# Performance work log

Measured on AMD Instinct MI355X. Metric: run time of the kernel, lower is better.

The kernel has to match this reference:

```python
import jax, jax.numpy as jnp
import numpy as np

HEAD_DEPTH = 64
CLIP = 10.0
SCALE = float(np.sqrt(HEAD_DEPTH))


def setup_inputs() -> dict:
    key = jax.random.key(0)
    kq, kk, kv, km = jax.random.split(key, 4)
    B, H, S, D = 4, 16, 2048, HEAD_DEPTH
    q = jax.random.normal(kq, (B, H, S, D), dtype=jnp.float32)
    k = jax.random.normal(kk, (B, H, S, D), dtype=jnp.float32)
    v = jax.random.normal(kv, (B, H, S, D), dtype=jnp.float32)
    # mask: (batch, n_nodes, 1) bool; True => key position is masked out
    mask = jax.random.randint(km, (B, S, 1), 0, 2).astype(bool)
    return {"q": q, "k": k, "v": v, "mask": mask}


def reference(q, k, v, mask):
    # logits: (B, H, Sq, Sk)
    logits = jnp.einsum('bhqd,bhkd->bhqk', q, k) / SCALE
    logits = CLIP * jnp.tanh(logits)  # tanh-clip of logits
    # mask (B, N, 1) -> broadcast over heads and query positions: (B, 1, 1, N)
    key_mask = mask[:, None, None, :, 0]
    logits = jnp.where(key_mask, -jnp.inf, logits)
    probs = jax.nn.softmax(logits, axis=-1)
    return jnp.einsum('bhqk,bhkd->bhqd', probs, v)
```

## Files before the change

### kernel.cpp

```cpp
#include <hip/hip_runtime.h>

typedef short bf16x8 __attribute__((ext_vector_type(8), may_alias));
typedef float f32x4 __attribute__((ext_vector_type(4)));
typedef unsigned int u32x4a __attribute__((ext_vector_type(4), may_alias));
typedef unsigned int u32x2a __attribute__((ext_vector_type(2), may_alias));
typedef unsigned short ushort;
typedef unsigned int uint;

#define B_N 4
#define H_N 16
#define S_N 2048
#define D_N 64
#define BQ 128
#define WQ 32
#define KT 64
#define NW 4
#define NBLK (B_N*H_N*(S_N/BQ))
#define TILE_BYTES 32768
#define MAXTILE (S_N/KT)
#define IMG_OFF 32768
#define WS_NEED ((size_t)IMG_OFF + (size_t)B_N*H_N*MAXTILE*TILE_BYTES)

#define MFMA16 __builtin_amdgcn_mfma_f32_16x16x32_bf16

__device__ __forceinline__ uint f2bf(float x){
  uint u = __float_as_uint(x);
  u += 0x7fffu + ((u >> 16) & 1u);
  return u >> 16;
}
__device__ __forceinline__ float bf2f(uint h){
  return __uint_as_float(h << 16);
}
__device__ __forceinline__ int ldsw(int off, int row){
  return off ^ ((row & 7) << 4);
}
__device__ __forceinline__ void gload16(const void* g, void* l){
  __builtin_amdgcn_global_load_lds((const uint __attribute__((address_space(1)))*)g,
                                   (uint __attribute__((address_space(3)))*)l, 16, 0, 0);
}

__global__ __launch_bounds__(256)
void compact_k(const int* __restrict__ Mg, int* __restrict__ cnt_ws,
               ushort* __restrict__ idx_ws)
{
  __shared__ int sws[NW];
  const int b = blockIdx.x;
  const int tid = threadIdx.x, lane = tid & 63, w = tid >> 6;
  const int* mb = Mg + (size_t)b * S_N;
  int kept[8]; int cl = 0; int base = tid * 8;
  #pragma unroll
  for (int i = 0; i < 8; ++i){ kept[i] = (mb[base+i] == 0); cl += kept[i]; }
  int inc = cl;
  #pragma unroll
  for (int d = 1; d < 64; d <<= 1){
    int o = __shfl_up(inc, d);
    if (lane >= d) inc += o;
  }
  if (lane == 63) sws[w] = inc;
  __syncthreads();
  int s0 = sws[0], s1 = sws[1], s2 = sws[2], s3 = sws[3];
  int wo = (w > 0 ? s0 : 0) + (w > 1 ? s1 : 0) + (w > 2 ? s2 : 0);
  int pos = wo + inc - cl;
  #pragma unroll
  for (int i = 0; i < 8; ++i){
    if (kept[i]) idx_ws[b*S_N + pos++] = (ushort)(base + i);
  }
  if (tid == 0) cnt_ws[b] = s0 + s1 + s2 + s3;
}

__global__ __launch_bounds__(256)
void stage_k(const float* __restrict__ Kg, const float* __restrict__ Vg,
             const int* __restrict__ cnt_ws, const ushort* __restrict__ idx_ws,
             char* __restrict__ img)
{
  __shared__ float Vl[64*65];
  const int bid = blockIdx.x;
  const int bh = bid >> 5;
  const int tile = bid & 31;
  const int b = bh >> 4;
  const int cnt = cnt_ws[b];
  const int ntile = (cnt + 63) >> 6;
  if (tile >= ntile) return;
  const int tid = threadIdx.x;
  char* G = img + (size_t)bid * TILE_BYTES;

  const int jrow = tid >> 2, c4 = tid & 3;
  int kk = tile*64 + jrow; if (kk >= cnt) kk = cnt - 1;
  const int sidx = idx_ws[b*S_N + kk];
  const size_t kvbase = (size_t)bh * (size_t)(S_N*D_N);
  const int sw = (jrow & 7) << 4;
  {
    const float4* Kp = (const float4*)(Kg + kvbase + (size_t)sidx*D_N) + c4*4;
    float4 k0 = Kp[0], k1 = Kp[1], k2 = Kp[2], k3 = Kp[3];
    float kv[16] = {k0.x,k0.y,k0.z,k0.w,k1.x,k1.y,k1.z,k1.w,
                    k2.x,k2.y,k2.z,k2.w,k3.x,k3.y,k3.z,k3.w};
    uint h[16], l[16];
    #pragma unroll
    for (int e = 0; e < 16; ++e){
      uint hh = f2bf(kv[e]); h[e] = hh; l[e] = f2bf(kv[e] - bf2f(hh));
    }
    char* r0 = G + jrow*128;
    char* r1 = G + 8192 + jrow*128;
    *(u32x4a*)(r0 + ((c4*32)      ^ sw)) = (u32x4a){h[0]|(h[1]<<16),  h[2]|(h[3]<<16),
                                                    h[4]|(h[5]<<16),  h[6]|(h[7]<<16)};
    *(u32x4a*)(r0 + ((c4*32 + 16) ^ sw)) = (u32x4a){h[8]|(h[9]<<16),  h[10]|(h[11]<<16),
                                                    h[12]|(h[13]<<16),h[14]|(h[15]<<16)};
    *(u32x4a*)(r1 + ((c4*32)      ^ sw)) = (u32x4a){l[0]|(l[1]<<16),  l[2]|(l[3]<<16),
                                                    l[4]|(l[5]<<16),  l[6]|(l[7]<<16)};
    *(u32x4a*)(r1 + ((c4*32 + 16) ^ sw)) = (u32x4a){l[8]|(l[9]<<16),  l[10]|(l[11]<<16),
                                                    l[12]|(l[13]<<16),l[14]|(l[15]<<16)};
  }
  {
    const float4* Vp = (const float4*)(Vg + kvbase + (size_t)sidx*D_N) + c4*4;
    float4 v0 = Vp[0], v1 = Vp[1], v2 = Vp[2], v3 = Vp[3];
    float vv[16] = {v0.x,v0.y,v0.z,v0.w,v1.x,v1.y,v1.z,v1.w,
                    v2.x,v2.y,v2.z,v2.w,v3.x,v3.y,v3.z,v3.w};
    #pragma unroll
    for (int e = 0; e < 16; ++e) Vl[jrow*65 + c4*16 + e] = vv[e];
  }
  __syncthreads();
  #pragma unroll
  for (int t = 0; t < 2; ++t){
    int idx2 = tid + t*256;
    int d = idx2 >> 3;
    int h = (idx2 >> 2) & 1;
    int g = idx2 & 3;
    int kb = h*32 + g*4;
    uint hh[8], ll[8];
    #pragma unroll
    for (int e = 0; e < 8; ++e){
      int k = kb + (e & 3) + ((e >> 2) << 4);
      float x = Vl[k*65 + d];
      uint hv = f2bf(x); hh[e] = hv; ll[e] = f2bf(x - bf2f(hv));
    }
    *(u32x4a*)(G + 16384 + d*128 + h*64 + g*16) =
        (u32x4a){hh[0]|(hh[1]<<16), hh[2]|(hh[3]<<16), hh[4]|(hh[5]<<16), hh[6]|(hh[7]<<16)};
    *(u32x4a*)(G + 24576 + d*128 + h*64 + g*16) =
        (u32x4a){ll[0]|(ll[1]<<16), ll[2]|(ll[3]<<16), ll[4]|(ll[5]<<16), ll[6]|(ll[7]<<16)};
  }
}

__global__ __launch_bounds__(256, 2)
void attn5_k(const float* __restrict__ Qg, const char* __restrict__ img,
             const int* __restrict__ cnt_ws, float* __restrict__ Og)
{
  __shared__ __align__(16) char smem[2][16384];

  const int tid  = threadIdx.x;
  const int lane = tid & 63;
  const int w    = tid >> 6;
  const int c    = lane & 15;
  const int gi   = lane >> 4;

  int bid = blockIdx.x;
  int wg  = (bid & 7) * (NBLK/8) + (bid >> 3);
  int qt  = wg & 15;
  int bh  = wg >> 4;
  int b   = bh >> 4;

  const int cnt = cnt_ws[b];
  const int nhalf = (cnt + 31) >> 5;
  const char* Gb = img + (size_t)bh * MAXTILE * TILE_BYTES;

  auto stage = [&](int hidx, int sb){
    const char* T = Gb + (size_t)(hidx >> 1) * TILE_BYTES;
    const int h = hidx & 1;
    char* Bse = (char*)&smem[sb][0];
    if (w < 2){
      const char* src = T + w*8192 + h*4096 + lane*16;
      char* dst = Bse + w*4096;
      #pragma unroll
      for (int i = 0; i < 4; ++i) gload16(src + i*1024, dst + i*1024);
    } else {
      const int hl = w - 2;
      const char* base = T + 16384 + hl*8192 + h*64;
      char* dst = Bse + 8192 + hl*4096;
      #pragma unroll
      for (int i = 0; i < 4; ++i){
        int pos = i*1024 + lane*16;
        int d = pos >> 6;
        int g = (pos >> 4) & 3;
        gload16(base + d*128 + g*16, dst + i*1024);
      }
    }
  };

  if (nhalf > 0) stage(0, 0);

  const int q0w = qt * BQ + w * WQ;
  bf16x8 qh[2][2], ql[2][2];
  {
    const float* Qbase = Qg + (size_t)bh * S_N * D_N;
    #pragma unroll
    for (int qs = 0; qs < 2; ++qs){
      const float* qr = Qbase + (size_t)(q0w + qs*16 + c) * D_N;
      #pragma unroll
      for (int ks = 0; ks < 2; ++ks){
        const float4* p4 = (const float4*)(qr + ks*32 + gi*8);
        float4 x0 = p4[0], x1 = p4[1];
        float xs[8] = {x0.x,x0.y,x0.z,x0.w,x1.x,x1.y,x1.z,x1.w};
        union { bf16x8 v; ushort u[8]; } uh, ul;
        #pragma unroll
        for (int e = 0; e < 8; ++e){
          uint h = f2bf(xs[e]);
          uh.u[e] = (ushort)h;
          ul.u[e] = (ushort)f2bf(xs[e] - bf2f(h));
        }
        qh[qs][ks] = uh.v; ql[qs][ks] = ul.v;
      }
    }
  }

  f32x4 Oa[2][4];
  #pragma unroll
  for (int i = 0; i < 2; ++i)
    #pragma unroll
    for (int jj = 0; jj < 4; ++jj)
      Oa[i][jj] = (f32x4){0.f,0.f,0.f,0.f};
  float zz[2] = {0.f, 0.f};

  const int swc16 = (c & 7) << 4;
  const int e0 = (gi*16) ^ swc16;
  const int e1 = (64 + gi*16) ^ swc16;

  __syncthreads();

  for (int tb = 0; tb < nhalf; ++tb){
    const int buf = tb & 1;
    if (tb + 1 < nhalf) stage(tb + 1, buf ^ 1);
    const char* Khi  = &smem[buf][0];
    const char* Klo  = Khi + 4096;
    const char* VThi = Khi + 8192;
    const char* VTlo = Khi + 12288;
    const bool lastt = (tb == nhalf - 1);

    uint sH[2][4], sL[2][4];
    #pragma unroll
    for (int kt = 0; kt < 2; ++kt){
      int row = kt*16 + c;
      const char* krh = Khi + row*128;
      const char* krl = Klo + row*128;
      bf16x8 kh0 = *(const bf16x8*)(krh + e0);
      bf16x8 kh1 = *(const bf16x8*)(krh + e1);
      bf16x8 kl0 = *(const bf16x8*)(krl + e0);
      bf16x8 kl1 = *(const bf16x8*)(krl + e1);
      #pragma unroll
      for (int qs = 0; qs < 2; ++qs){
        f32x4 s = (f32x4){0.f,0.f,0.f,0.f};
        s = MFMA16(kh0, qh[qs][0], s, 0,0,0);
        s = MFMA16(kh1, qh[qs][1], s, 0,0,0);
        s = MFMA16(kh0, ql[qs][0], s, 0,0,0);
        s = MFMA16(kh1, ql[qs][1], s, 0,0,0);
        s = MFMA16(kl0, qh[qs][0], s, 0,0,0);
        s = MFMA16(kl1, qh[qs][1], s, 0,0,0);
        float pv[4];
        #pragma unroll
        for (int r = 0; r < 4; ++r){
          float t  = __builtin_amdgcn_exp2f(s[r] * 0.3606737602222409f);
          float wv = __builtin_amdgcn_rcpf(t + 1.0f);
          pv[r] = __builtin_amdgcn_exp2f(-28.853900817779268f * wv);
        }
        if (lastt){
          int kg0 = tb*32 + kt*16 + gi*4;
          #pragma unroll
          for (int r = 0; r < 4; ++r) if (kg0 + r >= cnt) pv[r] = 0.f;
        }
        zz[qs] += (pv[0] + pv[1]) + (pv[2] + pv[3]);
        uint hA, hB, lA, lB;
        asm("v_cvt_pk_bf16_f32 %0, %1, %2" : "=v"(hA) : "v"(pv[0]), "v"(pv[1]));
        asm("v_cvt_pk_bf16_f32 %0, %1, %2" : "=v"(hB) : "v"(pv[2]), "v"(pv[3]));
        float l0 = pv[0] - __uint_as_float(hA << 16);
        float l1 = pv[1] - __uint_as_float(hA & 0xffff0000u);
        float l2 = pv[2] - __uint_as_float(hB << 16);
        float l3 = pv[3] - __uint_as_float(hB & 0xffff0000u);
        asm("v_cvt_pk_bf16_f32 %0, %1, %2" : "=v"(lA) : "v"(l0), "v"(l1));
        asm("v_cvt_pk_bf16_f32 %0, %1, %2" : "=v"(lB) : "v"(l2), "v"(l3));
        sH[qs][kt*2+0] = hA; sH[qs][kt*2+1] = hB;
        sL[qs][kt*2+0] = lA; sL[qs][kt*2+1] = lB;
      }
    }
    union PU { u32x4a g; bf16x8 v; };
    PU pah[2], pal[2];
    #pragma unroll
    for (int qs = 0; qs < 2; ++qs){
      pah[qs].g = (u32x4a){sH[qs][0], sH[qs][1], sH[qs][2], sH[qs][3]};
      pal[qs].g = (u32x4a){sL[qs][0], sL[qs][1], sL[qs][2], sL[qs][3]};
    }
    #pragma unroll
    for (int ds = 0; ds < 4; ++ds){
      int drow = ds*16 + c;
      bf16x8 vh = *(const bf16x8*)(VThi + drow*64 + gi*16);
      bf16x8 vl = *(const bf16x8*)(VTlo + drow*64 + gi*16);
      #pragma unroll
      for (int qs = 0; qs < 2; ++qs){
        f32x4 o = Oa[qs][ds];
        o = MFMA16(pah[qs].v, vh, o, 0,0,0);
        o = MFMA16(pah[qs].v, vl, o, 0,0,0);
        o = MFMA16(pal[qs].v, vh, o, 0,0,0);
        Oa[qs][ds] = o;
      }
    }
    __syncthreads();
  }

  #pragma unroll
  for (int qs = 0; qs < 2; ++qs){
    float zt = zz[qs];
    zt += __shfl_xor(zt, 16);
    zt += __shfl_xor(zt, 32);
    float rz = 1.0f / zt;
    #pragma unroll
    for (int r = 0; r < 4; ++r){
      float rzq = __shfl(rz, gi*4 + r);
      size_t rowbase = ((size_t)bh * S_N + (size_t)(q0w + qs*16 + gi*4 + r)) * D_N;
      #pragma unroll
      for (int ds = 0; ds < 4; ++ds){
        Og[rowbase + ds*16 + c] = Oa[qs][ds][r] * rzq;
      }
    }
  }
}

__global__ __launch_bounds__(256, 2)
void attn_k(const float* __restrict__ Qg, const float* __restrict__ Kg,
            const float* __restrict__ Vg, const int* __restrict__ Mg,
            float* __restrict__ Og)
{
  __shared__ __align__(16) ushort Khi[KT*D_N];
  __shared__ __align__(16) ushort Klo[KT*D_N];
  __shared__ __align__(16) ushort Vhi[D_N*72];
  __shared__ __align__(16) ushort Vlo[D_N*72];
  __shared__ __align__(16) ushort Phl[NW*16*72];
  __shared__ __align__(16) ushort Pll[NW*16*72];
  __shared__ ushort idx_l[S_N];
  __shared__ int scan_ws[NW];

  const int tid  = threadIdx.x;
  const int lane = tid & 63;
  const int w    = tid >> 6;
  const int c    = lane & 15;
  const int gi   = lane >> 4;

  int bid = blockIdx.x;
  int wg  = (bid & 7) * (NBLK/8) + (bid >> 3);
  int qt  = wg & 15;
  int bh  = wg >> 4;
  int b   = bh >> 4;

  int cnt;
  {
    const int* mb = Mg + (size_t)b * S_N;
    int kept[8]; int cl = 0;
    int base = tid * 8;
    #pragma unroll
    for (int i = 0; i < 8; ++i){ kept[i] = (mb[base+i] == 0); cl += kept[i]; }
    int inc = cl;
    #pragma unroll
    for (int d = 1; d < 64; d <<= 1){
      int o = __shfl_up(inc, d);
      if (lane >= d) inc += o;
    }
    if (lane == 63) scan_ws[w] = inc;
    __syncthreads();
    int s0 = scan_ws[0], s1 = scan_ws[1], s2 = scan_ws[2], s3 = scan_ws[3];
    int wo = (w > 0 ? s0 : 0) + (w > 1 ? s1 : 0) + (w > 2 ? s2 : 0);
    cnt = s0 + s1 + s2 + s3;
    int pos = wo + inc - cl;
    #pragma unroll
    for (int i = 0; i < 8; ++i){
      if (kept[i]) idx_l[pos++] = (ushort)(base + i);
    }
    __syncthreads();
  }

  const int q0w = qt * BQ + w * WQ;
  bf16x8 qh[2][2], ql[2][2];
  {
    const float* Qbase = Qg + (size_t)bh * S_N * D_N;
    #pragma unroll
    for (int qs = 0; qs < 2; ++qs){
      const float* qr = Qbase + (size_t)(q0w + qs*16 + c) * D_N;
      #pragma unroll
      for (int ks = 0; ks < 2; ++ks){
        const float4* p4 = (const float4*)(qr + ks*32 + gi*8);
        float4 x0 = p4[0], x1 = p4[1];
        float xs[8] = {x0.x,x0.y,x0.z,x0.w,x1.x,x1.y,x1.z,x1.w};
        union { bf16x8 v; ushort u[8]; } uh, ul;
        #pragma unroll
        for (int e = 0; e < 8; ++e){
          uint h = f2bf(xs[e]);
          uh.u[e] = (ushort)h;
          ul.u[e] = (ushort)f2bf(xs[e] - bf2f(h));
        }
        qh[qs][ks] = uh.v; ql[qs][ks] = ul.v;
      }
    }
  }

  f32x4 Oa[2][4];
  #pragma unroll
  for (int i = 0; i < 2; ++i)
    #pragma unroll
    for (int jj = 0; jj < 4; ++jj)
      Oa[i][jj] = (f32x4){0.f,0.f,0.f,0.f};
  float zz[2] = {0.f, 0.f};

  ushort* Ph = Phl + w * (16*72);
  ushort* Pl = Pll + w * (16*72);

  const int jrow = tid >> 2;
  const int c4   = tid & 3;
  const size_t kvbase = (size_t)bh * S_N * D_N;

  const int ntile = (cnt + KT - 1) >> 6;
  for (int tb = 0; tb < ntile; ++tb){
    {
      int kk = tb*KT + jrow;
      int ci = kk < cnt ? kk : cnt - 1;
      int sidx = idx_l[ci];
      const float4* Kp = (const float4*)(Kg + kvbase + (size_t)sidx * D_N) + c4*4;
      const float4* Vp = (const float4*)(Vg + kvbase + (size_t)sidx * D_N) + c4*4;
      float4 k0 = Kp[0], k1 = Kp[1], k2 = Kp[2], k3 = Kp[3];
      float kv[16] = {k0.x,k0.y,k0.z,k0.w,k1.x,k1.y,k1.z,k1.w,
                      k2.x,k2.y,k2.z,k2.w,k3.x,k3.y,k3.z,k3.w};
      uint kh[16], klv[16];
      #pragma unroll
      for (int e = 0; e < 16; ++e){
        uint h = f2bf(kv[e]);
        kh[e] = h; klv[e] = f2bf(kv[e] - bf2f(h));
      }
      u32x4a H0 = (u32x4a){kh[0]|(kh[1]<<16),   kh[2]|(kh[3]<<16),
                           kh[4]|(kh[5]<<16),   kh[6]|(kh[7]<<16)};
      u32x4a H1 = (u32x4a){kh[8]|(kh[9]<<16),   kh[10]|(kh[11]<<16),
                           kh[12]|(kh[13]<<16), kh[14]|(kh[15]<<16)};
      u32x4a L0 = (u32x4a){klv[0]|(klv[1]<<16),   klv[2]|(klv[3]<<16),
                           klv[4]|(klv[5]<<16),   klv[6]|(klv[7]<<16)};
      u32x4a L1 = (u32x4a){klv[8]|(klv[9]<<16),   klv[10]|(klv[11]<<16),
                           klv[12]|(klv[13]<<16), klv[14]|(klv[15]<<16)};
      char* krh = (char*)Khi + jrow*128;
      char* krl = (char*)Klo + jrow*128;
      int o0 = ldsw(c4*32, jrow), o1 = ldsw(c4*32 + 16, jrow);
      *(u32x4a*)(krh + o0) = H0;  *(u32x4a*)(krh + o1) = H1;
      *(u32x4a*)(krl + o0) = L0;  *(u32x4a*)(krl + o1) = L1;

      float4 v0 = Vp[0], v1 = Vp[1], v2 = Vp[2], v3 = Vp[3];
      float vv[16] = {v0.x,v0.y,v0.z,v0.w,v1.x,v1.y,v1.z,v1.w,
                      v2.x,v2.y,v2.z,v2.w,v3.x,v3.y,v3.z,v3.w};
      #pragma unroll
      for (int e = 0; e < 16; ++e){
        int d = c4*16 + e;
        uint h  = f2bf(vv[e]);
        uint l2 = f2bf(vv[e] - bf2f(h));
        int off = d*144 + ldsw(jrow*2, d);
        *(ushort*)((char*)Vhi + off) = (ushort)h;
        *(ushort*)((char*)Vlo + off) = (ushort)l2;
      }
    }
    __syncthreads();

    const bool lastt = (tb == ntile - 1);
    #pragma unroll
    for (int qs = 0; qs < 2; ++qs){
      #pragma unroll
      for (int kt = 0; kt < 4; ++kt){
        int row = kt*16 + c;
        const char* krh = (const char*)Khi + row*128;
        const char* krl = (const char*)Klo + row*128;
        int e0 = ldsw(16*gi, row), e1 = ldsw(64 + 16*gi, row);
        bf16x8 kh0 = *(const bf16x8*)(krh + e0);
        bf16x8 kh1 = *(const bf16x8*)(krh + e1);
        bf16x8 kl0 = *(const bf16x8*)(krl + e0);
        bf16x8 kl1 = *(const bf16x8*)(krl + e1);
        f32x4 s = (f32x4){0.f,0.f,0.f,0.f};
        s = MFMA16(kh0, qh[qs][0], s, 0,0,0);
        s = MFMA16(kh1, qh[qs][1], s, 0,0,0);
        s = MFMA16(kh0, ql[qs][0], s, 0,0,0);
        s = MFMA16(kh1, ql[qs][1], s, 0,0,0);
        s = MFMA16(kl0, qh[qs][0], s, 0,0,0);
        s = MFMA16(kl1, qh[qs][1], s, 0,0,0);
        float pv[4];
        #pragma unroll
        for (int r = 0; r < 4; ++r){
          float t  = __builtin_amdgcn_exp2f(s[r] * 0.3606737602222409f);
          float wv = __builtin_amdgcn_rcpf(t + 1.0f);
          pv[r] = __builtin_amdgcn_exp2f(-28.853900817779268f * wv);
        }
        if (lastt){
          int kg0 = tb*KT + kt*16 + gi*4;
          #pragma unroll
          for (int r = 0; r < 4; ++r) if (kg0 + r >= cnt) pv[r] = 0.f;
        }
        zz[qs] += (pv[0] + pv[1]) + (pv[2] + pv[3]);
        uint h0 = f2bf(pv[0]), h1 = f2bf(pv[1]),
             h2 = f2bf(pv[2]), h3 = f2bf(pv[3]);
        uint l0 = f2bf(pv[0]-bf2f(h0)), l1 = f2bf(pv[1]-bf2f(h1)),
             l2 = f2bf(pv[2]-bf2f(h2)), l3 = f2bf(pv[3]-bf2f(h3));
        int ow = c*144 + ldsw(kt*32 + gi*8, c);
        *(u32x2a*)((char*)Ph + ow) = (u32x2a){h0|(h1<<16), h2|(h3<<16)};
        *(u32x2a*)((char*)Pl + ow) = (u32x2a){l0|(l1<<16), l2|(l3<<16)};
      }
      bf16x8 pah[2], pal[2];
      {
        const char* prh = (const char*)Ph + c*144;
        const char* prl = (const char*)Pl + c*144;
        #pragma unroll
        for (int ks = 0; ks < 2; ++ks){
          int oo = ldsw(64*ks + 16*gi, c);
          pah[ks] = *(const bf16x8*)(prh + oo);
          pal[ks] = *(const bf16x8*)(prl + oo);
        }
      }
      #pragma unroll
      for (int ds = 0; ds < 4; ++ds){
        int drow = ds*16 + c;
        const char* vrh = (const char*)Vhi + drow*144;
        const char* vrl = (const char*)Vlo + drow*144;
        f32x4 o = Oa[qs][ds];
        #pragma unroll
        for (int ks = 0; ks < 2; ++ks){
          int oo = ldsw(64*ks + 16*gi, drow);
          bf16x8 vh = *(const bf16x8*)(vrh + oo);
          bf16x8 vl = *(const bf16x8*)(vrl + oo);
          o = MFMA16(pah[ks], vh, o, 0,0,0);
          o = MFMA16(pah[ks], vl, o, 0,0,0);
          o = MFMA16(pal[ks], vh, o, 0,0,0);
        }
        Oa[qs][ds] = o;
      }
    }
    __syncthreads();
  }

  #pragma unroll
  for (int qs = 0; qs < 2; ++qs){
    float zt = zz[qs];
    zt += __shfl_xor(zt, 16);
    zt += __shfl_xor(zt, 32);
    float rz = 1.0f / zt;
    #pragma unroll
    for (int r = 0; r < 4; ++r){
      float rzq = __shfl(rz, gi*4 + r);
      size_t rowbase = ((size_t)bh * S_N + (size_t)(q0w + qs*16 + gi*4 + r)) * D_N;
      #pragma unroll
      for (int ds = 0; ds < 4; ++ds){
        Og[rowbase + ds*16 + c] = Oa[qs][ds][r] * rzq;
      }
    }
  }
}

extern "C" void kernel_launch(void* const* d_in, const int* in_sizes, int n_in,
                              void* d_out, int out_size, void* d_ws, size_t ws_size,
                              hipStream_t stream) {
  const float* Qg = (const float*)d_in[0];
  const float* Kg = (const float*)d_in[1];
  const float* Vg = (const float*)d_in[2];
  const int*   Mg = (const int*)d_in[3];
  float* Og = (float*)d_out;
  if (ws_size >= WS_NEED){
    int*    cnt_ws = (int*)d_ws;
    ushort* idx_ws = (ushort*)((char*)d_ws + 64);
    char*   img    = (char*)d_ws + IMG_OFF;
    compact_k<<<dim3(B_N), dim3(256), 0, stream>>>(Mg, cnt_ws, idx_ws);
    stage_k<<<dim3(B_N*H_N*MAXTILE), dim3(256), 0, stream>>>(Kg, Vg, cnt_ws, idx_ws, img);
    attn5_k<<<dim3(NBLK), dim3(256), 0, stream>>>(Qg, img, cnt_ws, Og);
  } else {
    attn_k<<<dim3(NBLK), dim3(256), 0, stream>>>(Qg, Kg, Vg, Mg, Og);
  }
}
```

Baseline: 137.2 us.

## Read K/V fragments directly from global in MFMA-ready layout, drop LDS staging

The staged K/V image is rewritten into a fragment-major layout, so each lane's bf16x8 MFMA operand sits contiguously and a wave's loads are coalesced 16-byte reads. The attention kernel then loads K and V fragments straight from global memory (relying on L2/cache reuse across the 4 waves and 16 query tiles) instead of double-buffering through LDS with global_load_lds and per-tile barriers. This removes LDS traffic and the __syncthreads, at the cost of each wave issuing its own global loads, with latency no longer hidden by async prefetch.

```diff
diff --git a/kernel.cpp b/kernel.cpp
--- a/kernel.cpp
+++ b/kernel.cpp
@@ -33,10 +33,6 @@
 }
 __device__ __forceinline__ int ldsw(int off, int row){
   return off ^ ((row & 7) << 4);
-}
-__device__ __forceinline__ void gload16(const void* g, void* l){
-  __builtin_amdgcn_global_load_lds((const uint __attribute__((address_space(1)))*)g,
-                                   (uint __attribute__((address_space(3)))*)l, 16, 0, 0);
 }
 
 __global__ __launch_bounds__(256)
@@ -88,7 +84,6 @@
   int kk = tile*64 + jrow; if (kk >= cnt) kk = cnt - 1;
   const int sidx = idx_ws[b*S_N + kk];
   const size_t kvbase = (size_t)bh * (size_t)(S_N*D_N);
-  const int sw = (jrow & 7) << 4;
   {
     const float4* Kp = (const float4*)(Kg + kvbase + (size_t)sidx*D_N) + c4*4;
     float4 k0 = Kp[0], k1 = Kp[1], k2 = Kp[2], k3 = Kp[3];
@@ -99,16 +94,15 @@
     for (int e = 0; e < 16; ++e){
       uint hh = f2bf(kv[e]); h[e] = hh; l[e] = f2bf(kv[e] - bf2f(hh));
     }
-    char* r0 = G + jrow*128;
-    char* r1 = G + 8192 + jrow*128;
-    *(u32x4a*)(r0 + ((c4*32)      ^ sw)) = (u32x4a){h[0]|(h[1]<<16),  h[2]|(h[3]<<16),
-                                                    h[4]|(h[5]<<16),  h[6]|(h[7]<<16)};
-    *(u32x4a*)(r0 + ((c4*32 + 16) ^ sw)) = (u32x4a){h[8]|(h[9]<<16),  h[10]|(h[11]<<16),
-                                                    h[12]|(h[13]<<16),h[14]|(h[15]<<16)};
-    *(u32x4a*)(r1 + ((c4*32)      ^ sw)) = (u32x4a){l[0]|(l[1]<<16),  l[2]|(l[3]<<16),
-                                                    l[4]|(l[5]<<16),  l[6]|(l[7]<<16)};
-    *(u32x4a*)(r1 + ((c4*32 + 16) ^ sw)) = (u32x4a){l[8]|(l[9]<<16),  l[10]|(l[11]<<16),
-                                                    l[12]|(l[13]<<16),l[14]|(l[15]<<16)};
+    const int g0 = c4*2, g1 = c4*2 + 1;
+    *(u32x4a*)(G + g0*1024 + jrow*16) = (u32x4a){h[0]|(h[1]<<16),  h[2]|(h[3]<<16),
+                                                 h[4]|(h[5]<<16),  h[6]|(h[7]<<16)};
+    *(u32x4a*)(G + g1*1024 + jrow*16) = (u32x4a){h[8]|(h[9]<<16),  h[10]|(h[11]<<16),
+                                                 h[12]|(h[13]<<16),h[14]|(h[15]<<16)};
+    *(u32x4a*)(G + 8192 + g0*1024 + jrow*16) = (u32x4a){l[0]|(l[1]<<16),  l[2]|(l[3]<<16),
+                                                        l[4]|(l[5]<<16),  l[6]|(l[7]<<16)};
+    *(u32x4a*)(G + 8192 + g1*1024 + jrow*16) = (u32x4a){l[8]|(l[9]<<16),  l[10]|(l[11]<<16),
+                                                        l[12]|(l[13]<<16),l[14]|(l[15]<<16)};
   }
   {
     const float4* Vp = (const float4*)(Vg + kvbase + (size_t)sidx*D_N) + c4*4;
@@ -133,19 +127,17 @@
       float x = Vl[k*65 + d];
       uint hv = f2bf(x); hh[e] = hv; ll[e] = f2bf(x - bf2f(hv));
     }
-    *(u32x4a*)(G + 16384 + d*128 + h*64 + g*16) =
+    *(u32x4a*)(G + 16384 + g*2048 + h*1024 + d*16) =
         (u32x4a){hh[0]|(hh[1]<<16), hh[2]|(hh[3]<<16), hh[4]|(hh[5]<<16), hh[6]|(hh[7]<<16)};
-    *(u32x4a*)(G + 24576 + d*128 + h*64 + g*16) =
+    *(u32x4a*)(G + 24576 + g*2048 + h*1024 + d*16) =
         (u32x4a){ll[0]|(ll[1]<<16), ll[2]|(ll[3]<<16), ll[4]|(ll[5]<<16), ll[6]|(ll[7]<<16)};
   }
 }
 
 __global__ __launch_bounds__(256, 2)
-void attn5_k(const float* __restrict__ Qg, const char* __restrict__ img,
+void attn6_k(const float* __restrict__ Qg, const char* __restrict__ img,
              const int* __restrict__ cnt_ws, float* __restrict__ Og)
 {
-  __shared__ __align__(16) char smem[2][16384];
-
   const int tid  = threadIdx.x;
   const int lane = tid & 63;
   const int w    = tid >> 6;
@@ -161,31 +153,6 @@
   const int cnt = cnt_ws[b];
   const int nhalf = (cnt + 31) >> 5;
   const char* Gb = img + (size_t)bh * MAXTILE * TILE_BYTES;
-
-  auto stage = [&](int hidx, int sb){
-    const char* T = Gb + (size_t)(hidx >> 1) * TILE_BYTES;
-    const int h = hidx & 1;
-    char* Bse = (char*)&smem[sb][0];
-    if (w < 2){
-      const char* src = T + w*8192 + h*4096 + lane*16;
-      char* dst = Bse + w*4096;
-      #pragma unroll
-      for (int i = 0; i < 4; ++i) gload16(src + i*1024, dst + i*1024);
-    } else {
-      const int hl = w - 2;
-      const char* base = T + 16384 + hl*8192 + h*64;
-      char* dst = Bse + 8192 + hl*4096;
-      #pragma unroll
-      for (int i = 0; i < 4; ++i){
-        int pos = i*1024 + lane*16;
-        int d = pos >> 6;
-        int g = (pos >> 4) & 3;
-        gload16(base + d*128 + g*16, dst + i*1024);
-      }
-    }
-  };
-
-  if (nhalf > 0) stage(0, 0);
 
   const int q0w = qt * BQ + w * WQ;
   bf16x8 qh[2][2], ql[2][2];
@@ -219,31 +186,19 @@
       Oa[i][jj] = (f32x4){0.f,0.f,0.f,0.f};
   float zz[2] = {0.f, 0.f};
 
-  const int swc16 = (c & 7) << 4;
-  const int e0 = (gi*16) ^ swc16;
-  const int e1 = (64 + gi*16) ^ swc16;
-
-  __syncthreads();
-
   for (int tb = 0; tb < nhalf; ++tb){
-    const int buf = tb & 1;
-    if (tb + 1 < nhalf) stage(tb + 1, buf ^ 1);
-    const char* Khi  = &smem[buf][0];
-    const char* Klo  = Khi + 4096;
-    const char* VThi = Khi + 8192;
-    const char* VTlo = Khi + 12288;
+    const char* T  = Gb + (size_t)(tb >> 1) * TILE_BYTES;
+    const char* KB = T + gi*1024 + ((tb & 1)*32 + c)*16;
+    const char* VB = T + 16384 + gi*2048 + (tb & 1)*1024 + c*16;
     const bool lastt = (tb == nhalf - 1);
 
     uint sH[2][4], sL[2][4];
     #pragma unroll
     for (int kt = 0; kt < 2; ++kt){
-      int row = kt*16 + c;
-      const char* krh = Khi + row*128;
-      const char* krl = Klo + row*128;
-      bf16x8 kh0 = *(const bf16x8*)(krh + e0);
-      bf16x8 kh1 = *(const bf16x8*)(krh + e1);
-      bf16x8 kl0 = *(const bf16x8*)(krl + e0);
-      bf16x8 kl1 = *(const bf16x8*)(krl + e1);
+      bf16x8 kh0 = *(const bf16x8*)(KB + kt*256);
+      bf16x8 kh1 = *(const bf16x8*)(KB + 4096 + kt*256);
+      bf16x8 kl0 = *(const bf16x8*)(KB + 8192 + kt*256);
+      bf16x8 kl1 = *(const bf16x8*)(KB + 12288 + kt*256);
       #pragma unroll
       for (int qs = 0; qs < 2; ++qs){
         f32x4 s = (f32x4){0.f,0.f,0.f,0.f};
@@ -288,9 +243,8 @@
     }
     #pragma unroll
     for (int ds = 0; ds < 4; ++ds){
-      int drow = ds*16 + c;
-      bf16x8 vh = *(const bf16x8*)(VThi + drow*64 + gi*16);
-      bf16x8 vl = *(const bf16x8*)(VTlo + drow*64 + gi*16);
+      bf16x8 vh = *(const bf16x8*)(VB + ds*256);
+      bf16x8 vl = *(const bf16x8*)(VB + 8192 + ds*256);
       #pragma unroll
       for (int qs = 0; qs < 2; ++qs){
         f32x4 o = Oa[qs][ds];
@@ -300,7 +254,6 @@
         Oa[qs][ds] = o;
       }
     }
-    __syncthreads();
   }
 
   #pragma unroll
@@ -563,7 +516,7 @@
     char*   img    = (char*)d_ws + IMG_OFF;
     compact_k<<<dim3(B_N), dim3(256), 0, stream>>>(Mg, cnt_ws, idx_ws);
     stage_k<<<dim3(B_N*H_N*MAXTILE), dim3(256), 0, stream>>>(Kg, Vg, cnt_ws, idx_ws, img);
-    attn5_k<<<dim3(NBLK), dim3(256), 0, stream>>>(Qg, img, cnt_ws, Og);
+    attn6_k<<<dim3(NBLK), dim3(256), 0, stream>>>(Qg, img, cnt_ws, Og);
   } else {
     attn_k<<<dim3(NBLK), dim3(256), 0, stream>>>(Qg, Kg, Vg, Mg, Og);
   }
```

Result: slower. 149.2 us (+8.8%).

## Read V operands directly from global memory in MFMA layout, skip LDS staging

Applied to the files above, without the earlier changes.

The staging kernel now writes V^T hi/lo into a layout that matches the per-lane MFMA operand order. The attention kernel then loads V fragments straight from global memory (through cache) instead of copying them into shared memory. Only K is double-buffered in LDS, which halves shared memory per block and removes half of the async copies. The cost is that V loads become global-latency reads inside the inner loop with no prefetch, and every wave re-reads the same V data from cache.

```diff
diff --git a/kernel.cpp b/kernel.cpp
--- a/kernel.cpp
+++ b/kernel.cpp
@@ -133,18 +133,18 @@
       float x = Vl[k*65 + d];
       uint hv = f2bf(x); hh[e] = hv; ll[e] = f2bf(x - bf2f(hv));
     }
-    *(u32x4a*)(G + 16384 + d*128 + h*64 + g*16) =
+    *(u32x4a*)(G + 16384 + g*2048 + h*1024 + d*16) =
         (u32x4a){hh[0]|(hh[1]<<16), hh[2]|(hh[3]<<16), hh[4]|(hh[5]<<16), hh[6]|(hh[7]<<16)};
-    *(u32x4a*)(G + 24576 + d*128 + h*64 + g*16) =
+    *(u32x4a*)(G + 24576 + g*2048 + h*1024 + d*16) =
         (u32x4a){ll[0]|(ll[1]<<16), ll[2]|(ll[3]<<16), ll[4]|(ll[5]<<16), ll[6]|(ll[7]<<16)};
   }
 }
 
 __global__ __launch_bounds__(256, 2)
-void attn5_k(const float* __restrict__ Qg, const char* __restrict__ img,
+void attn9_k(const float* __restrict__ Qg, const char* __restrict__ img,
              const int* __restrict__ cnt_ws, float* __restrict__ Og)
 {
-  __shared__ __align__(16) char smem[2][16384];
+  __shared__ __align__(16) char smem[2][8192];
 
   const int tid  = threadIdx.x;
   const int lane = tid & 63;
@@ -163,25 +163,13 @@
   const char* Gb = img + (size_t)bh * MAXTILE * TILE_BYTES;
 
   auto stage = [&](int hidx, int sb){
-    const char* T = Gb + (size_t)(hidx >> 1) * TILE_BYTES;
-    const int h = hidx & 1;
-    char* Bse = (char*)&smem[sb][0];
     if (w < 2){
+      const char* T = Gb + (size_t)(hidx >> 1) * TILE_BYTES;
+      const int h = hidx & 1;
       const char* src = T + w*8192 + h*4096 + lane*16;
-      char* dst = Bse + w*4096;
+      char* dst = (char*)&smem[sb][0] + w*4096;
       #pragma unroll
       for (int i = 0; i < 4; ++i) gload16(src + i*1024, dst + i*1024);
-    } else {
-      const int hl = w - 2;
-      const char* base = T + 16384 + hl*8192 + h*64;
-      char* dst = Bse + 8192 + hl*4096;
-      #pragma unroll
-      for (int i = 0; i < 4; ++i){
-        int pos = i*1024 + lane*16;
-        int d = pos >> 6;
-        int g = (pos >> 4) & 3;
-        gload16(base + d*128 + g*16, dst + i*1024);
-      }
     }
   };
 
@@ -230,8 +218,8 @@
     if (tb + 1 < nhalf) stage(tb + 1, buf ^ 1);
     const char* Khi  = &smem[buf][0];
     const char* Klo  = Khi + 4096;
-    const char* VThi = Khi + 8192;
-    const char* VTlo = Khi + 12288;
+    const char* VB = Gb + (size_t)(tb >> 1) * TILE_BYTES + 16384
+                     + gi*2048 + (tb & 1)*1024 + c*16;
     const bool lastt = (tb == nhalf - 1);
 
     uint sH[2][4], sL[2][4];
@@ -288,9 +276,8 @@
     }
     #pragma unroll
     for (int ds = 0; ds < 4; ++ds){
-      int drow = ds*16 + c;
-      bf16x8 vh = *(const bf16x8*)(VThi + drow*64 + gi*16);
-      bf16x8 vl = *(const bf16x8*)(VTlo + drow*64 + gi*16);
+      bf16x8 vh = *(const bf16x8*)(VB + ds*256);
+      bf16x8 vl = *(const bf16x8*)(VB + 8192 + ds*256);
       #pragma unroll
       for (int qs = 0; qs < 2; ++qs){
         f32x4 o = Oa[qs][ds];
@@ -563,7 +550,7 @@
     char*   img    = (char*)d_ws + IMG_OFF;
     compact_k<<<dim3(B_N), dim3(256), 0, stream>>>(Mg, cnt_ws, idx_ws);
     stage_k<<<dim3(B_N*H_N*MAXTILE), dim3(256), 0, stream>>>(Kg, Vg, cnt_ws, idx_ws, img);
-    attn5_k<<<dim3(NBLK), dim3(256), 0, stream>>>(Qg, img, cnt_ws, Og);
+    attn9_k<<<dim3(NBLK), dim3(256), 0, stream>>>(Qg, img, cnt_ws, Og);
   } else {
     attn_k<<<dim3(NBLK), dim3(256), 0, stream>>>(Qg, Kg, Vg, Mg, Og);
   }
```

Measured after the change: 167.6 us. +22.1%, slower.

## Process full 64-key tiles per iteration with swizzled V^T staging in LDS

Applied to the files above, without the earlier changes.

The attention loop now consumes a whole 64-key staged tile per iteration instead of a 32-key half tile. This halves the number of loop trips and barriers, and each staging call issues twice as many async global-to-LDS loads. The V^T copy is XOR-swizzled on load so the wider 128-byte rows avoid LDS bank conflicts. Shared memory per block doubles to 64KB, and the score and packed-probability register arrays double, which may limit occupancy or cause spills under the 2-blocks launch bound. Masking of the last partial tile now uses 64-key granularity, so more wasted work on the tail.

```diff
diff --git a/kernel.cpp b/kernel.cpp
--- a/kernel.cpp
+++ b/kernel.cpp
@@ -141,10 +141,10 @@
 }
 
 __global__ __launch_bounds__(256, 2)
-void attn5_k(const float* __restrict__ Qg, const char* __restrict__ img,
-             const int* __restrict__ cnt_ws, float* __restrict__ Og)
+void attn13_k(const float* __restrict__ Qg, const char* __restrict__ img,
+              const int* __restrict__ cnt_ws, float* __restrict__ Og)
 {
-  __shared__ __align__(16) char smem[2][16384];
+  __shared__ __align__(16) char smem[2][32768];
 
   const int tid  = threadIdx.x;
   const int lane = tid & 63;
@@ -159,33 +159,32 @@
   int b   = bh >> 4;
 
   const int cnt = cnt_ws[b];
-  const int nhalf = (cnt + 31) >> 5;
+  const int ntile = (cnt + 63) >> 6;
   const char* Gb = img + (size_t)bh * MAXTILE * TILE_BYTES;
 
-  auto stage = [&](int hidx, int sb){
-    const char* T = Gb + (size_t)(hidx >> 1) * TILE_BYTES;
-    const int h = hidx & 1;
+  auto stage = [&](int t, int sb){
+    const char* T = Gb + (size_t)t * TILE_BYTES;
     char* Bse = (char*)&smem[sb][0];
     if (w < 2){
-      const char* src = T + w*8192 + h*4096 + lane*16;
-      char* dst = Bse + w*4096;
-      #pragma unroll
-      for (int i = 0; i < 4; ++i) gload16(src + i*1024, dst + i*1024);
+      const char* src = T + w*8192 + lane*16;
+      char* dst = Bse + w*8192;
+      #pragma unroll
+      for (int i = 0; i < 8; ++i) gload16(src + i*1024, dst + i*1024);
     } else {
       const int hl = w - 2;
-      const char* base = T + 16384 + hl*8192 + h*64;
-      char* dst = Bse + 8192 + hl*4096;
-      #pragma unroll
-      for (int i = 0; i < 4; ++i){
+      const char* base = T + 16384 + hl*8192;
+      char* dst = Bse + 16384 + hl*8192;
+      #pragma unroll
+      for (int i = 0; i < 8; ++i){
         int pos = i*1024 + lane*16;
-        int d = pos >> 6;
-        int g = (pos >> 4) & 3;
-        gload16(base + d*128 + g*16, dst + i*1024);
+        int d = pos >> 7;
+        int off = pos & 127;
+        gload16(base + d*128 + (off ^ ((d & 7) << 4)), dst + i*1024);
       }
     }
   };
 
-  if (nhalf > 0) stage(0, 0);
+  if (ntile > 0) stage(0, 0);
 
   const int q0w = qt * BQ + w * WQ;
   bf16x8 qh[2][2], ql[2][2];
@@ -225,18 +224,18 @@
 
   __syncthreads();
 
-  for (int tb = 0; tb < nhalf; ++tb){
+  for (int tb = 0; tb < ntile; ++tb){
     const int buf = tb & 1;
-    if (tb + 1 < nhalf) stage(tb + 1, buf ^ 1);
+    if (tb + 1 < ntile) stage(tb + 1, buf ^ 1);
     const char* Khi  = &smem[buf][0];
-    const char* Klo  = Khi + 4096;
-    const char* VThi = Khi + 8192;
-    const char* VTlo = Khi + 12288;
-    const bool lastt = (tb == nhalf - 1);
-
-    uint sH[2][4], sL[2][4];
-    #pragma unroll
-    for (int kt = 0; kt < 2; ++kt){
+    const char* Klo  = Khi + 8192;
+    const char* VThi = Khi + 16384;
+    const char* VTlo = Khi + 24576;
+    const bool lastt = (tb == ntile - 1);
+
+    uint sH[2][8], sL[2][8];
+    #pragma unroll
+    for (int kt = 0; kt < 4; ++kt){
       int row = kt*16 + c;
       const char* krh = Khi + row*128;
       const char* krl = Klo + row*128;
@@ -261,7 +260,7 @@
           pv[r] = __builtin_amdgcn_exp2f(-28.853900817779268f * wv);
         }
         if (lastt){
-          int kg0 = tb*32 + kt*16 + gi*4;
+          int kg0 = tb*64 + kt*16 + gi*4;
           #pragma unroll
           for (int r = 0; r < 4; ++r) if (kg0 + r >= cnt) pv[r] = 0.f;
         }
@@ -280,24 +279,33 @@
       }
     }
     union PU { u32x4a g; bf16x8 v; };
-    PU pah[2], pal[2];
+    PU pah[2][2], pal[2][2];
     #pragma unroll
     for (int qs = 0; qs < 2; ++qs){
-      pah[qs].g = (u32x4a){sH[qs][0], sH[qs][1], sH[qs][2], sH[qs][3]};
-      pal[qs].g = (u32x4a){sL[qs][0], sL[qs][1], sL[qs][2], sL[qs][3]};
+      #pragma unroll
+      for (int h = 0; h < 2; ++h){
+        pah[qs][h].g = (u32x4a){sH[qs][4*h+0], sH[qs][4*h+1], sH[qs][4*h+2], sH[qs][4*h+3]};
+        pal[qs][h].g = (u32x4a){sL[qs][4*h+0], sL[qs][4*h+1], sL[qs][4*h+2], sL[qs][4*h+3]};
+      }
     }
     #pragma unroll
     for (int ds = 0; ds < 4; ++ds){
       int drow = ds*16 + c;
-      bf16x8 vh = *(const bf16x8*)(VThi + drow*64 + gi*16);
-      bf16x8 vl = *(const bf16x8*)(VTlo + drow*64 + gi*16);
-      #pragma unroll
-      for (int qs = 0; qs < 2; ++qs){
-        f32x4 o = Oa[qs][ds];
-        o = MFMA16(pah[qs].v, vh, o, 0,0,0);
-        o = MFMA16(pah[qs].v, vl, o, 0,0,0);
-        o = MFMA16(pal[qs].v, vh, o, 0,0,0);
-        Oa[qs][ds] = o;
+      const char* vbh = VThi + drow*128;
+      const char* vbl = VTlo + drow*128;
+      #pragma unroll
+      for (int h = 0; h < 2; ++h){
+        int vo = (h*64 + gi*16) ^ swc16;
+        bf16x8 vh = *(const bf16x8*)(vbh + vo);
+        bf16x8 vl = *(const bf16x8*)(vbl + vo);
+        #pragma unroll
+        for (int qs = 0; qs < 2; ++qs){
+          f32x4 o = Oa[qs][ds];
+          o = MFMA16(pah[qs][h].v, vh, o, 0,0,0);
+          o = MFMA16(pah[qs][h].v, vl, o, 0,0,0);
+          o = MFMA16(pal[qs][h].v, vh, o, 0,0,0);
+          Oa[qs][ds] = o;
+        }
       }
     }
     __syncthreads();
@@ -563,7 +571,7 @@
     char*   img    = (char*)d_ws + IMG_OFF;
     compact_k<<<dim3(B_N), dim3(256), 0, stream>>>(Mg, cnt_ws, idx_ws);
     stage_k<<<dim3(B_N*H_N*MAXTILE), dim3(256), 0, stream>>>(Kg, Vg, cnt_ws, idx_ws, img);
-    attn5_k<<<dim3(NBLK), dim3(256), 0, stream>>>(Qg, img, cnt_ws, Og);
+    attn13_k<<<dim3(NBLK), dim3(256), 0, stream>>>(Qg, img, cnt_ws, Og);
   } else {
     attn_k<<<dim3(NBLK), dim3(256), 0, stream>>>(Qg, Kg, Vg, Mg, Og);
   }
```

New measurement: 133.7 us, median of 2. 2.5% less time.
